# Optimization experiments

Hardware: AMD Instinct MI355X
Metric: run time of the kernel (lower is better)

The kernel has to match this reference:

```python
import jax, jax.numpy as jnp
import numpy as np


def setup_inputs() -> dict:
    key = jax.random.key(0)
    ks = jax.random.split(key, 7)
    B, C, H, W = 16, 256, 1, 4096
    x = jax.random.normal(ks[0], (B, C, H, W), dtype=jnp.float32)
    init = lambda k, s: jax.random.normal(k, s, dtype=jnp.float32) * 0.02
    return {
        "x": x,
        "Wq": init(ks[1], (C, C)), "bq": jnp.zeros((C,), jnp.float32),
        "Wk": init(ks[2], (C, C)), "bk": jnp.zeros((C,), jnp.float32),
        "Wv": init(ks[3], (C, C)), "bv": jnp.zeros((C,), jnp.float32),
    }


def reference(x, Wq, bq, Wk, bk, Wv, bv):
    B, C, H, W = x.shape
    xs = jnp.transpose(x[:, :, 0, :], (0, 2, 1))  # [B, W, C]
    Q = xs @ Wq.T + bq  # [B, W, C]
    K = xs @ Wk.T + bk
    V = xs @ Wv.T + bv
    scale = jnp.sqrt(jnp.asarray(C, dtype=Q.dtype))

    # radius-1 sliding window along width; pad so window gather is static
    Kp = jnp.pad(K, ((0, 0), (1, 1), (0, 0)))  # [B, W+2, C]
    Vp = jnp.pad(V, ((0, 0), (1, 1), (0, 0)))
    idx = jnp.arange(W)[:, None] + jnp.arange(3)[None, :]  # padded indices [W,3]
    pos = idx - 1  # original positions (may be -1 or W -> invalid at edges)
    valid = (pos >= 0) & (pos < W)  # [W, 3]

    Kw = Kp[:, idx]  # [B, W, 3, C]
    Vw = Vp[:, idx]  # [B, W, 3, C]

    scores = jnp.einsum('bwc,bwkc->bwk', Q, Kw) / scale  # [B, W, 3]
    scores = jnp.where(valid[None], scores, jnp.asarray(-1e9, scores.dtype))
    attn = jax.nn.softmax(scores, axis=-1)
    out = jnp.einsum('bwk,bwkc->bwc', attn, Vw)  # [B, W, C]
    # [B, W, C] -> [B, C, 1, W]
    return jnp.transpose(out, (0, 2, 1))[:, :, None, :]
```

## Files before the change

### kernel.cpp

```cpp
#include <hip/hip_runtime.h>
#include <hip/hip_bf16.h>

#define C_DIM 256
#define W_DIM 4096
#define LDS_BYTES 162528

typedef unsigned short u16;
typedef short s16x8 __attribute__((ext_vector_type(8)));
typedef unsigned short u16x8 __attribute__((ext_vector_type(8)));
typedef unsigned short u16x4 __attribute__((ext_vector_type(4)));
typedef float f32x16 __attribute__((ext_vector_type(16)));

__device__ __forceinline__ u16 f2b(float f) {
  return __builtin_bit_cast(u16, __float2bfloat16(f));
}
__device__ __forceinline__ float b2f(u16 u) {
  return __builtin_bit_cast(float, ((unsigned)u) << 16);
}

__global__ __launch_bounds__(256) void prep_kernel(
    const float* __restrict__ Wq, const float* __restrict__ bq,
    const float* __restrict__ Wk, const float* __restrict__ bk,
    const float* __restrict__ Wv, char* __restrict__ ws) {
  u16* Mb   = (u16*)ws;
  u16* Wvb  = (u16*)(ws + 131072);
  float* u0 = (float*)(ws + 262144);
  float* u1 = (float*)(ws + 263168);
  float* c0p = (float*)(ws + 264192);
  int bid = blockIdx.x, t = threadIdx.x;
  if (bid < 256) {
    __shared__ float Wqs[256*17];
    __shared__ float Wks[256*17];
    int i0 = (bid >> 4) << 4, j0 = (bid & 15) << 4;
    for (int it = 0; it < 16; ++it) {
      int e = t + 256*it; int a = e >> 4, ii = e & 15;
      Wqs[a*17+ii] = Wq[a*256 + i0 + ii];
      Wks[a*17+ii] = Wk[a*256 + j0 + ii];
    }
    __syncthreads();
    int ii = t >> 4, jj = t & 15;
    float acc = 0.f;
    #pragma unroll 8
    for (int a = 0; a < 256; ++a) acc += Wqs[a*17+ii] * Wks[a*17+jj];
    Mb[(i0+ii)*256 + j0 + jj] = f2b(acc);
  } else if (bid == 256) {
    int j = t;
    float a0 = 0.f, a1 = 0.f;
    #pragma unroll 4
    for (int a = 0; a < 256; ++a) {
      a0 += bq[a] * Wk[a*256 + j];
      a1 += bk[a] * Wq[a*256 + j];
    }
    u0[j] = a0; u1[j] = a1;
    __shared__ float red[256];
    red[t] = bq[t] * bk[t];
    __syncthreads();
    if (t == 0) { float s = 0.f; for (int a = 0; a < 256; ++a) s += red[a]; *c0p = s; }
  } else {
    int base = ((bid - 257)*256 + t) * 4;
    const float4 v = *reinterpret_cast<const float4*>(Wv + base);
    ushort4 pk = make_ushort4(f2b(v.x), f2b(v.y), f2b(v.z), f2b(v.w));
    *reinterpret_cast<ushort4*>(Wvb + base) = pk;
  }
}

__global__ __launch_bounds__(1024, 4) void main_kernel(
    const float* __restrict__ x, const char* __restrict__ ws,
    const float* __restrict__ bv, float* __restrict__ out) {
  const u16* Mb   = (const u16*)ws;
  const u16* Wvb  = (const u16*)(ws + 131072);
  const float* u0g = (const float*)(ws + 262144);
  const float* u1g = (const float*)(ws + 263168);
  const float c0  = *(const float*)(ws + 264192);

  extern __shared__ char lds[];
  u16*   Xt  = (u16*)lds;
  float* Ps  = (float*)(lds + 132608);
  float* ABs = (float*)(lds + 157376);
  float* fS  = (float*)(lds + 159440);
  float* U   = (float*)(lds + 159456);
  float* bvs = (float*)(lds + 161504);

  const int bid = blockIdx.x;
  const int t = threadIdx.x;
  const int wv = t >> 6, l = t & 63;
  const int col = l & 31, half = l >> 5;
  const int rg = wv & 7, nh = wv >> 3;
  const int nbase = 4*nh;
  const int kkA = 2*wv;

  const int b  = bid >> 4;
  const int cw = bid & 15;
  const int w0 = cw << 8;
  const float* xb = x + (size_t)b * (C_DIM*W_DIM);
  float* outb = out + (size_t)b * (C_DIM*W_DIM);

  for (int i = t; i < 6192; i += 1024) Ps[i] = 0.f;
  if (t < 4) fS[t] = 0.f;
  if (t < 256) { U[t] = u0g[t]; U[256+t] = u1g[t]; bvs[t] = bv[t]; }
  __syncthreads();

  {
    #pragma unroll
    for (int p = 0; p < 4; ++p) {
      int j = 64*p + l;
      int w = w0 - 1 + j;
      bool ok = (w >= 0);
      const float* xp = xb + w;
      float xr[16];
      #pragma unroll
      for (int g2 = 0; g2 < 2; ++g2)
        #pragma unroll
        for (int e = 0; e < 8; ++e)
          xr[g2*8+e] = ok ? xp[(size_t)((kkA+g2)*8 + e) * W_DIM] : 0.f;
      float pa = 0.f, pb_ = 0.f;
      #pragma unroll
      for (int g2 = 0; g2 < 2; ++g2) {
        int kk = kkA + g2;
        union { u16 u[8]; u16x8 v; } pk;
        #pragma unroll
        for (int e = 0; e < 8; ++e) {
          float v = xr[g2*8+e];
          pk.u[e] = f2b(v);
          int c = kk*8 + e;
          pa  += U[c] * v;
          pb_ += U[256 + c] * v;
        }
        *reinterpret_cast<u16x8*>(Xt + (kk*259 + j)*8) = pk.v;
      }
      atomicAdd(&Ps[rg*258 + j], pa);
      atomicAdd(&Ps[2064 + rg*258 + j], pb_);
    }
    if (l < 3) {
      int j = 256 + l;
      int w = w0 - 1 + j;
      bool real = (l < 2) && (w < W_DIM);
      const float* xpe = xb + w;
      float pa = 0.f, pb_ = 0.f;
      #pragma unroll
      for (int g2 = 0; g2 < 2; ++g2) {
        int kk = kkA + g2;
        union { u16 u[8]; u16x8 v; } pk;
        #pragma unroll
        for (int e = 0; e < 8; ++e) {
          float v = real ? xpe[(size_t)(kk*8+e) * W_DIM] : 0.f;
          pk.u[e] = f2b(v);
          int c = kk*8 + e;
          pa  += U[c] * v;
          pb_ += U[256 + c] * v;
        }
        *reinterpret_cast<u16x8*>(Xt + (kk*259 + j)*8) = pk.v;
      }
      if (l < 2) {
        atomicAdd(&Ps[rg*258 + j], pa);
        atomicAdd(&Ps[2064 + rg*258 + j], pb_);
      }
    }
  }
  __syncthreads();

  f32x16 acc[4];
  #pragma unroll
  for (int ni = 0; ni < 4; ++ni)
    #pragma unroll
    for (int r = 0; r < 16; ++r) acc[ni][r] = 0.f;
  {
    const u16* Arow = Mb + (32*rg + col)*256 + 8*half;
    #pragma unroll
    for (int kk = 0; kk < 16; ++kk) {
      s16x8 a = *reinterpret_cast<const s16x8*>(Arow + 16*kk);
      const u16* Bb = Xt + (2*kk + half)*259*8;
      #pragma unroll
      for (int ni = 0; ni < 4; ++ni) {
        s16x8 bfr = *reinterpret_cast<const s16x8*>(Bb + (32*(nbase+ni) + col)*8);
        acc[ni] = __builtin_amdgcn_mfma_f32_32x32x16_bf16(a, bfr, acc[ni], 0, 0, 0);
      }
    }
  }

  {
    int i = t >> 2, kq = t & 3;
    float xi255 = b2f(Xt[((i>>3)*259 + 255)*8 + (i&7)]);
    float xi256 = b2f(Xt[((i>>3)*259 + 256)*8 + (i&7)]);
    float a1 = 0.f, a2 = 0.f;
    const u16* Mrow = Mb + i*256 + 64*kq;
    #pragma unroll
    for (int kk8 = 0; kk8 < 8; ++kk8) {
      int sA = 8*kq + kk8;
      s16x8 m8 = *reinterpret_cast<const s16x8*>(Mrow + 8*kk8);
      u16x8 xk6 = *reinterpret_cast<const u16x8*>(Xt + (sA*259 + 256)*8);
      u16x8 xk7 = *reinterpret_cast<const u16x8*>(Xt + (sA*259 + 257)*8);
      #pragma unroll
      for (int e = 0; e < 8; ++e) {
        float m = b2f((u16)m8[e]);
        a1 += m * b2f(xk6[e]);
        a2 += m * b2f(xk7[e]);
      }
    }
    float p1 = xi256*a1, p2 = xi256*a2, p3 = xi255*a1;
    #pragma unroll
    for (int d = 1; d < 64; d <<= 1) {
      p1 += __shfl_xor(p1, d); p2 += __shfl_xor(p2, d); p3 += __shfl_xor(p3, d);
    }
    if (l == 0) { atomicAdd(&fS[0], p1); atomicAdd(&fS[1], p2); atomicAdd(&fS[2], p3); }
  }
  for (int i = t; i < 516; i += 1024) {
    int which = (i >= 258) ? 1 : 0;
    int jj = i - 258*which;
    float s = 0.f;
    #pragma unroll
    for (int g = 0; g < 8; ++g) s += Ps[which*2064 + g*258 + jj];
    ABs[which*258 + jj] = s;
  }
  __syncthreads();

  {
    #pragma unroll
    for (int ni = 0; ni < 4; ++ni) {
      int jt = 32*(nbase+ni) + col;
      int jm = (jt > 0) ? jt-1 : 0;
      int jp = jt + 1;
      float s0 = 0.f, s1 = 0.f, s2 = 0.f;
      #pragma unroll
      for (int q = 0; q < 4; ++q) {
        const u16* base = Xt + (4*rg + q)*259*8 + 4*half;
        u16x4 xm = *reinterpret_cast<const u16x4*>(base + jm*8);
        u16x4 xc = *reinterpret_cast<const u16x4*>(base + jt*8);
        u16x4 xp = *reinterpret_cast<const u16x4*>(base + jp*8);
        #pragma unroll
        for (int r4 = 0; r4 < 4; ++r4) {
          float g0 = acc[ni][4*q + r4];
          s2 += g0 * b2f(xm[r4]);
          s1 += g0 * b2f(xc[r4]);
          s0 += g0 * b2f(xp[r4]);
        }
      }
      s0 += __shfl_xor(s0, 32);
      s1 += __shfl_xor(s1, 32);
      s2 += __shfl_xor(s2, 32);
      if (half == 0) {
        Ps[0*2064 + rg*258 + jt+1] = s0;
        if (jt >= 1) Ps[1*2064 + rg*258 + jt]   = s1;
        if (jt >= 2) Ps[2*2064 + rg*258 + jt-1] = s2;
      }
    }
  }
  __syncthreads();

  {
    float aw0[4], aw1[4], aw2[4];
    #pragma unroll
    for (int p = 0; p < 4; ++p) {
      int oc = 64*p + l;
      int jp = oc + 1;
      float d0 = 0.f, d1 = 0.f, d2 = 0.f;
      #pragma unroll
      for (int g = 0; g < 8; ++g) {
        d0 += Ps[0*2064 + g*258 + jp];
        d1 += Ps[1*2064 + g*258 + jp];
        d2 += Ps[2*2064 + g*258 + jp];
      }
      if (oc == 255)      { d1 = fS[0]; d2 = fS[1]; }
      else if (oc == 254) { d2 = fS[2]; }
      float am = ABs[jp-1], ac_ = ABs[jp], ap_ = ABs[jp+1];
      float be = ABs[258 + jp];
      float sc0 = (d0 + am + be + c0) * 0.0625f;
      float sc1 = (d1 + ac_ + be + c0) * 0.0625f;
      float sc2 = (d2 + ap_ + be + c0) * 0.0625f;
      int w = w0 + oc;
      bool v0 = (w >= 1), v2 = (w + 1 < W_DIM);
      const float NEG = -1e30f;
      float m = fmaxf(v0 ? sc0 : NEG, fmaxf(sc1, v2 ? sc2 : NEG));
      float e0v = v0 ? __expf(sc0 - m) : 0.f;
      float e1v = __expf(sc1 - m);
      float e2v = v2 ? __expf(sc2 - m) : 0.f;
      float inv = 1.f / (e0v + e1v + e2v);
      aw0[p] = e0v*inv; aw1[p] = e1v*inv; aw2[p] = e2v*inv;
    }
    #pragma unroll
    for (int g2 = 0; g2 < 2; ++g2) {
      u16* base = Xt + (kkA + g2)*259*8;
      u16x8 xrd[12];
      #pragma unroll
      for (int p = 0; p < 4; ++p)
        #pragma unroll
        for (int i = 0; i < 3; ++i)
          xrd[p*3+i] = *reinterpret_cast<const u16x8*>(base + (64*p + l + i)*8);
      __builtin_amdgcn_sched_barrier(0);
      #pragma unroll
      for (int p = 0; p < 4; ++p) {
        union { u16 u[8]; u16x8 v; } pk;
        #pragma unroll
        for (int e = 0; e < 8; ++e)
          pk.u[e] = f2b(aw0[p]*b2f(xrd[p*3][e]) + aw1[p]*b2f(xrd[p*3+1][e])
                        + aw2[p]*b2f(xrd[p*3+2][e]));
        *reinterpret_cast<u16x8*>(base + (64*p + l + 1)*8) = pk.v;
      }
      __builtin_amdgcn_sched_barrier(0);
    }
  }
  __syncthreads();

  {
    #pragma unroll
    for (int ni = 0; ni < 4; ++ni)
      #pragma unroll
      for (int r = 0; r < 16; ++r) acc[ni][r] = 0.f;
    const u16* Arow2 = Wvb + (32*rg + col)*256 + 8*half;
    #pragma unroll
    for (int kk = 0; kk < 16; ++kk) {
      s16x8 a = *reinterpret_cast<const s16x8*>(Arow2 + 16*kk);
      const u16* Bb = Xt + (2*kk + half)*259*8;
      #pragma unroll
      for (int ni = 0; ni < 4; ++ni) {
        s16x8 bfr = *reinterpret_cast<const s16x8*>(Bb + (1 + 32*(nbase+ni) + col)*8);
        acc[ni] = __builtin_amdgcn_mfma_f32_32x32x16_bf16(a, bfr, acc[ni], 0, 0, 0);
      }
    }
    float bvr[16];
    #pragma unroll
    for (int q = 0; q < 4; ++q) {
      const float4 t4 = *reinterpret_cast<const float4*>(bvs + 32*rg + 8*q + 4*half);
      bvr[4*q+0] = t4.x; bvr[4*q+1] = t4.y; bvr[4*q+2] = t4.z; bvr[4*q+3] = t4.w;
    }
    #pragma unroll
    for (int ni = 0; ni < 4; ++ni)
      #pragma unroll
      for (int r = 0; r < 16; ++r) {
        int crow = 32*rg + (r&3) + 8*(r>>2) + 4*half;
        outb[(size_t)crow*W_DIM + w0 + 32*(nbase+ni) + col] = acc[ni][r] + bvr[r];
      }
  }
}

extern "C" void kernel_launch(void* const* d_in, const int* in_sizes, int n_in,
                              void* d_out, int out_size, void* d_ws, size_t ws_size,
                              hipStream_t stream) {
  (void)in_sizes; (void)n_in; (void)out_size; (void)ws_size;
  const float* x  = (const float*)d_in[0];
  const float* Wq = (const float*)d_in[1];
  const float* bq = (const float*)d_in[2];
  const float* Wk = (const float*)d_in[3];
  const float* bk = (const float*)d_in[4];
  const float* Wv = (const float*)d_in[5];
  const float* bv = (const float*)d_in[6];
  float* out = (float*)d_out;
  char* ws = (char*)d_ws;

  hipFuncSetAttribute((const void*)main_kernel,
                      hipFuncAttributeMaxDynamicSharedMemorySize, LDS_BYTES);
  prep_kernel<<<321, 256, 0, stream>>>(Wq, bq, Wk, bk, Wv, ws);
  main_kernel<<<256, 1024, LDS_BYTES, stream>>>(x, ws, bv, out);
}
```

Before: 87.93 us.

## Halve block size to 512 threads with 2x MFMA row tiles per wave

Main kernel now uses 8 waves instead of 16. Each wave computes two 32-row MFMA tiles that share one B fragment, and loads four channel groups of x instead of two. With 8 waves, each wave now writes its own partial-sum slot, so the LDS atomics and the Ps zeroing are removed. The change cuts LDS traffic for B fragments and the atomics, at the cost of fewer waves to hide latency, given that the LDS footprint already limits the kernel to one block per CU.

```diff
diff --git a/kernel.cpp b/kernel.cpp
--- a/kernel.cpp
+++ b/kernel.cpp
@@ -64,7 +64,7 @@
   }
 }
 
-__global__ __launch_bounds__(1024, 4) void main_kernel(
+__global__ __launch_bounds__(512, 2) void main_kernel(
     const float* __restrict__ x, const char* __restrict__ ws,
     const float* __restrict__ bv, float* __restrict__ out) {
   const u16* Mb   = (const u16*)ws;
@@ -85,9 +85,7 @@
   const int t = threadIdx.x;
   const int wv = t >> 6, l = t & 63;
   const int col = l & 31, half = l >> 5;
-  const int rg = wv & 7, nh = wv >> 3;
-  const int nbase = 4*nh;
-  const int kkA = 2*wv;
+  const int rs = wv & 3, cs = wv >> 2;
 
   const int b  = bid >> 4;
   const int cw = bid & 15;
@@ -95,7 +93,6 @@
   const float* xb = x + (size_t)b * (C_DIM*W_DIM);
   float* outb = out + (size_t)b * (C_DIM*W_DIM);
 
-  for (int i = t; i < 6192; i += 1024) Ps[i] = 0.f;
   if (t < 4) fS[t] = 0.f;
   if (t < 256) { U[t] = u0g[t]; U[256+t] = u1g[t]; bvs[t] = bv[t]; }
   __syncthreads();
@@ -107,29 +104,28 @@
       int w = w0 - 1 + j;
       bool ok = (w >= 0);
       const float* xp = xb + w;
-      float xr[16];
-      #pragma unroll
-      for (int g2 = 0; g2 < 2; ++g2)
+      float xr[32];
+      #pragma unroll
+      for (int g = 0; g < 4; ++g)
         #pragma unroll
         for (int e = 0; e < 8; ++e)
-          xr[g2*8+e] = ok ? xp[(size_t)((kkA+g2)*8 + e) * W_DIM] : 0.f;
+          xr[g*8+e] = ok ? xp[(size_t)((4*wv+g)*8 + e) * W_DIM] : 0.f;
       float pa = 0.f, pb_ = 0.f;
       #pragma unroll
-      for (int g2 = 0; g2 < 2; ++g2) {
-        int kk = kkA + g2;
+      for (int g = 0; g < 4; ++g) {
+        int kk = 4*wv + g;
         union { u16 u[8]; u16x8 v; } pk;
         #pragma unroll
         for (int e = 0; e < 8; ++e) {
-          float v = xr[g2*8+e];
+          float v = xr[g*8+e];
           pk.u[e] = f2b(v);
-          int c = kk*8 + e;
-          pa  += U[c] * v;
-          pb_ += U[256 + c] * v;
+          pa  += U[kk*8+e] * v;
+          pb_ += U[256 + kk*8+e] * v;
         }
         *reinterpret_cast<u16x8*>(Xt + (kk*259 + j)*8) = pk.v;
       }
-      atomicAdd(&Ps[rg*258 + j], pa);
-      atomicAdd(&Ps[2064 + rg*258 + j], pb_);
+      Ps[wv*258 + j] = pa;
+      Ps[2064 + wv*258 + j] = pb_;
     }
     if (l < 3) {
       int j = 256 + l;
@@ -138,55 +134,57 @@
       const float* xpe = xb + w;
       float pa = 0.f, pb_ = 0.f;
       #pragma unroll
-      for (int g2 = 0; g2 < 2; ++g2) {
-        int kk = kkA + g2;
+      for (int g = 0; g < 4; ++g) {
+        int kk = 4*wv + g;
         union { u16 u[8]; u16x8 v; } pk;
         #pragma unroll
         for (int e = 0; e < 8; ++e) {
           float v = real ? xpe[(size_t)(kk*8+e) * W_DIM] : 0.f;
           pk.u[e] = f2b(v);
-          int c = kk*8 + e;
-          pa  += U[c] * v;
-          pb_ += U[256 + c] * v;
+          pa  += U[kk*8+e] * v;
+          pb_ += U[256 + kk*8+e] * v;
         }
         *reinterpret_cast<u16x8*>(Xt + (kk*259 + j)*8) = pk.v;
       }
       if (l < 2) {
-        atomicAdd(&Ps[rg*258 + j], pa);
-        atomicAdd(&Ps[2064 + rg*258 + j], pb_);
-      }
-    }
-  }
-  __syncthreads();
-
-  f32x16 acc[4];
+        Ps[wv*258 + j] = pa;
+        Ps[2064 + wv*258 + j] = pb_;
+      }
+    }
+  }
+  __syncthreads();
+
+  f32x16 acc0[4], acc1[4];
   #pragma unroll
   for (int ni = 0; ni < 4; ++ni)
     #pragma unroll
-    for (int r = 0; r < 16; ++r) acc[ni][r] = 0.f;
-  {
-    const u16* Arow = Mb + (32*rg + col)*256 + 8*half;
+    for (int r = 0; r < 16; ++r) { acc0[ni][r] = 0.f; acc1[ni][r] = 0.f; }
+  {
+    const u16* Arow0 = Mb + (64*rs + col)*256 + 8*half;
+    const u16* Arow1 = Arow0 + 32*256;
     #pragma unroll
     for (int kk = 0; kk < 16; ++kk) {
-      s16x8 a = *reinterpret_cast<const s16x8*>(Arow + 16*kk);
+      s16x8 a0 = *reinterpret_cast<const s16x8*>(Arow0 + 16*kk);
+      s16x8 a1 = *reinterpret_cast<const s16x8*>(Arow1 + 16*kk);
       const u16* Bb = Xt + (2*kk + half)*259*8;
       #pragma unroll
       for (int ni = 0; ni < 4; ++ni) {
-        s16x8 bfr = *reinterpret_cast<const s16x8*>(Bb + (32*(nbase+ni) + col)*8);
-        acc[ni] = __builtin_amdgcn_mfma_f32_32x32x16_bf16(a, bfr, acc[ni], 0, 0, 0);
-      }
-    }
-  }
-
-  {
-    int i = t >> 2, kq = t & 3;
+        s16x8 bfr = *reinterpret_cast<const s16x8*>(Bb + (32*(4*cs+ni) + col)*8);
+        acc0[ni] = __builtin_amdgcn_mfma_f32_32x32x16_bf16(a0, bfr, acc0[ni], 0, 0, 0);
+        acc1[ni] = __builtin_amdgcn_mfma_f32_32x32x16_bf16(a1, bfr, acc1[ni], 0, 0, 0);
+      }
+    }
+  }
+
+  {
+    int i = t >> 1, kq = t & 1;
     float xi255 = b2f(Xt[((i>>3)*259 + 255)*8 + (i&7)]);
     float xi256 = b2f(Xt[((i>>3)*259 + 256)*8 + (i&7)]);
     float a1 = 0.f, a2 = 0.f;
-    const u16* Mrow = Mb + i*256 + 64*kq;
-    #pragma unroll
-    for (int kk8 = 0; kk8 < 8; ++kk8) {
-      int sA = 8*kq + kk8;
+    const u16* Mrow = Mb + i*256 + 128*kq;
+    #pragma unroll
+    for (int kk8 = 0; kk8 < 16; ++kk8) {
+      int sA = 16*kq + kk8;
       s16x8 m8 = *reinterpret_cast<const s16x8*>(Mrow + 8*kk8);
       u16x8 xk6 = *reinterpret_cast<const u16x8*>(Xt + (sA*259 + 256)*8);
       u16x8 xk7 = *reinterpret_cast<const u16x8*>(Xt + (sA*259 + 257)*8);
@@ -204,7 +202,7 @@
     }
     if (l == 0) { atomicAdd(&fS[0], p1); atomicAdd(&fS[1], p2); atomicAdd(&fS[2], p3); }
   }
-  for (int i = t; i < 516; i += 1024) {
+  for (int i = t; i < 516; i += 512) {
     int which = (i >= 258) ? 1 : 0;
     int jj = i - 258*which;
     float s = 0.f;
@@ -216,32 +214,37 @@
 
   {
     #pragma unroll
-    for (int ni = 0; ni < 4; ++ni) {
-      int jt = 32*(nbase+ni) + col;
-      int jm = (jt > 0) ? jt-1 : 0;
-      int jp = jt + 1;
-      float s0 = 0.f, s1 = 0.f, s2 = 0.f;
-      #pragma unroll
-      for (int q = 0; q < 4; ++q) {
-        const u16* base = Xt + (4*rg + q)*259*8 + 4*half;
-        u16x4 xm = *reinterpret_cast<const u16x4*>(base + jm*8);
-        u16x4 xc = *reinterpret_cast<const u16x4*>(base + jt*8);
-        u16x4 xp = *reinterpret_cast<const u16x4*>(base + jp*8);
-        #pragma unroll
-        for (int r4 = 0; r4 < 4; ++r4) {
-          float g0 = acc[ni][4*q + r4];
-          s2 += g0 * b2f(xm[r4]);
-          s1 += g0 * b2f(xc[r4]);
-          s0 += g0 * b2f(xp[r4]);
+    for (int rt = 0; rt < 2; ++rt) {
+      const int rg = 2*rs + rt;
+      #pragma unroll
+      for (int ni = 0; ni < 4; ++ni) {
+        int jt = 32*(4*cs+ni) + col;
+        int jm = (jt > 0) ? jt-1 : 0;
+        int jp = jt + 1;
+        float s0 = 0.f, s1 = 0.f, s2 = 0.f;
+        #pragma unroll
+        for (int q = 0; q < 4; ++q) {
+          const u16* base = Xt + (4*rg + q)*259*8 + 4*half;
+          u16x4 xm = *reinterpret_cast<const u16x4*>(base + jm*8);
+          u16x4 xc = *reinterpret_cast<const u16x4*>(base + jt*8);
+          u16x4 xp = *reinterpret_cast<const u16x4*>(base + jp*8);
+          const f32x16& A = rt ? acc1[ni] : acc0[ni];
+          #pragma unroll
+          for (int r4 = 0; r4 < 4; ++r4) {
+            float g0 = A[4*q + r4];
+            s2 += g0 * b2f(xm[r4]);
+            s1 += g0 * b2f(xc[r4]);
+            s0 += g0 * b2f(xp[r4]);
+          }
         }
-      }
-      s0 += __shfl_xor(s0, 32);
-      s1 += __shfl_xor(s1, 32);
-      s2 += __shfl_xor(s2, 32);
-      if (half == 0) {
-        Ps[0*2064 + rg*258 + jt+1] = s0;
-        if (jt >= 1) Ps[1*2064 + rg*258 + jt]   = s1;
-        if (jt >= 2) Ps[2*2064 + rg*258 + jt-1] = s2;
+        s0 += __shfl_xor(s0, 32);
+        s1 += __shfl_xor(s1, 32);
+        s2 += __shfl_xor(s2, 32);
+        if (half == 0) {
+          Ps[0*2064 + rg*258 + jt+1] = s0;
+          if (jt >= 1) Ps[1*2064 + rg*258 + jt]   = s1;
+          if (jt >= 2) Ps[2*2064 + rg*258 + jt-1] = s2;
+        }
       }
     }
   }
@@ -278,8 +281,8 @@
       aw0[p] = e0v*inv; aw1[p] = e1v*inv; aw2[p] = e2v*inv;
     }
     #pragma unroll
-    for (int g2 = 0; g2 < 2; ++g2) {
-      u16* base = Xt + (kkA + g2)*259*8;
+    for (int g = 0; g < 4; ++g) {
+      u16* base = Xt + (4*wv + g)*259*8;
       u16x8 xrd[12];
       #pragma unroll
       for (int p = 0; p < 4; ++p)
@@ -305,30 +308,31 @@
     #pragma unroll
     for (int ni = 0; ni < 4; ++ni)
       #pragma unroll
-      for (int r = 0; r < 16; ++r) acc[ni][r] = 0.f;
-    const u16* Arow2 = Wvb + (32*rg + col)*256 + 8*half;
+      for (int r = 0; r < 16; ++r) { acc0[ni][r] = 0.f; acc1[ni][r] = 0.f; }
+    const u16* Arow0 = Wvb + (64*rs + col)*256 + 8*half;
+    const u16* Arow1 = Arow0 + 32*256;
     #pragma unroll
     for (int kk = 0; kk < 16; ++kk) {
-      s16x8 a = *reinterpret_cast<const s16x8*>(Arow2 + 16*kk);
+      s16x8 a0 = *reinterpret_cast<const s16x8*>(Arow0 + 16*kk);
+      s16x8 a1 = *reinterpret_cast<const s16x8*>(Arow1 + 16*kk);
       const u16* Bb = Xt + (2*kk + half)*259*8;
       #pragma unroll
       for (int ni = 0; ni < 4; ++ni) {
-        s16x8 bfr = *reinterpret_cast<const s16x8*>(Bb + (1 + 32*(nbase+ni) + col)*8);
-        acc[ni] = __builtin_amdgcn_mfma_f32_32x32x16_bf16(a, bfr, acc[ni], 0, 0, 0);
-      }
-    }
-    float bvr[16];
-    #pragma unroll
-    for (int q = 0; q < 4; ++q) {
-      const float4 t4 = *reinterpret_cast<const float4*>(bvs + 32*rg + 8*q + 4*half);
-      bvr[4*q+0] = t4.x; bvr[4*q+1] = t4.y; bvr[4*q+2] = t4.z; bvr[4*q+3] = t4.w;
+        s16x8 bfr = *reinterpret_cast<const s16x8*>(Bb + (1 + 32*(4*cs+ni) + col)*8);
+        acc0[ni] = __builtin_amdgcn_mfma_f32_32x32x16_bf16(a0, bfr, acc0[ni], 0, 0, 0);
+        acc1[ni] = __builtin_amdgcn_mfma_f32_32x32x16_bf16(a1, bfr, acc1[ni], 0, 0, 0);
+      }
     }
     #pragma unroll
     for (int ni = 0; ni < 4; ++ni)
       #pragma unroll
       for (int r = 0; r < 16; ++r) {
-        int crow = 32*rg + (r&3) + 8*(r>>2) + 4*half;
-        outb[(size_t)crow*W_DIM + w0 + 32*(nbase+ni) + col] = acc[ni][r] + bvr[r];
+        int rloc = (r&3) + 8*(r>>2) + 4*half;
+        int crow0 = 64*rs + rloc;
+        int crow1 = crow0 + 32;
+        int oc = 32*(4*cs+ni) + col;
+        outb[(size_t)crow0*W_DIM + w0 + oc] = acc0[ni][r] + bvs[crow0];
+        outb[(size_t)crow1*W_DIM + w0 + oc] = acc1[ni][r] + bvs[crow1];
       }
   }
 }
@@ -350,5 +354,5 @@
   hipFuncSetAttribute((const void*)main_kernel,
                       hipFuncAttributeMaxDynamicSharedMemorySize, LDS_BYTES);
   prep_kernel<<<321, 256, 0, stream>>>(Wq, bq, Wk, bk, Wv, ws);
-  main_kernel<<<256, 1024, LDS_BYTES, stream>>>(x, ws, bv, out);
-}
+  main_kernel<<<256, 512, LDS_BYTES, stream>>>(x, ws, bv, out);
+}
```

New measurement: 84.43 us. -4.0%, faster.

## Halve width tile to 128 columns with 512-thread blocks and smaller LDS

Applied to the files above, without the earlier changes.

Each block now covers 128 width columns with 8 waves instead of 256 columns with 16 waves, so the grid doubles to 512 blocks and LDS use drops to about 77 KB. Each wave now owns a full 32-row channel slice across all four column tiles. Partial-sum buffers move from per-wave writes to atomic adds over 4 groups, with an extra zeroing pass and barrier. The aim is better occupancy (two blocks per CU fit in LDS) and more blocks to spread across CUs. The cost is twice as many halo columns and tail-correction computations, plus more LDS atomics.

```diff
diff --git a/kernel.cpp b/kernel.cpp
--- a/kernel.cpp
+++ b/kernel.cpp
@@ -3,7 +3,8 @@
 
 #define C_DIM 256
 #define W_DIM 4096
-#define LDS_BYTES 162528
+#define LDS_BYTES 76928
+#define XROW 1040
 
 typedef unsigned short u16;
 typedef short s16x8 __attribute__((ext_vector_type(8)));
@@ -64,7 +65,7 @@
   }
 }
 
-__global__ __launch_bounds__(1024, 4) void main_kernel(
+__global__ __launch_bounds__(512, 4) void main_kernel(
     const float* __restrict__ x, const char* __restrict__ ws,
     const float* __restrict__ bv, float* __restrict__ out) {
   const u16* Mb   = (const u16*)ws;
@@ -75,86 +76,84 @@
 
   extern __shared__ char lds[];
   u16*   Xt  = (u16*)lds;
-  float* Ps  = (float*)(lds + 132608);
-  float* ABs = (float*)(lds + 157376);
-  float* fS  = (float*)(lds + 159440);
-  float* U   = (float*)(lds + 159456);
-  float* bvs = (float*)(lds + 161504);
+  float* Ps  = (float*)(lds + 66560);
+  float* ABs = (float*)(lds + 72800);
+  float* fS  = (float*)(lds + 73840);
+  float* U   = (float*)(lds + 73856);
+  float* bvs = (float*)(lds + 75904);
 
   const int bid = blockIdx.x;
   const int t = threadIdx.x;
   const int wv = t >> 6, l = t & 63;
   const int col = l & 31, half = l >> 5;
-  const int rg = wv & 7, nh = wv >> 3;
-  const int nbase = 4*nh;
-  const int kkA = 2*wv;
-
-  const int b  = bid >> 4;
-  const int cw = bid & 15;
-  const int w0 = cw << 8;
+  const int g4 = wv & 3;
+  const int kkA = 4*wv;
+
+  const int b  = bid >> 5;
+  const int cw = bid & 31;
+  const int w0 = cw << 7;
   const float* xb = x + (size_t)b * (C_DIM*W_DIM);
   float* outb = out + (size_t)b * (C_DIM*W_DIM);
 
-  for (int i = t; i < 6192; i += 1024) Ps[i] = 0.f;
+  for (int i = t; i < 1560; i += 512) Ps[i] = 0.f;
   if (t < 4) fS[t] = 0.f;
   if (t < 256) { U[t] = u0g[t]; U[256+t] = u1g[t]; bvs[t] = bv[t]; }
   __syncthreads();
 
   {
     #pragma unroll
-    for (int p = 0; p < 4; ++p) {
+    for (int p = 0; p < 2; ++p) {
       int j = 64*p + l;
       int w = w0 - 1 + j;
       bool ok = (w >= 0);
       const float* xp = xb + w;
-      float xr[16];
-      #pragma unroll
-      for (int g2 = 0; g2 < 2; ++g2)
-        #pragma unroll
-        for (int e = 0; e < 8; ++e)
-          xr[g2*8+e] = ok ? xp[(size_t)((kkA+g2)*8 + e) * W_DIM] : 0.f;
       float pa = 0.f, pb_ = 0.f;
       #pragma unroll
-      for (int g2 = 0; g2 < 2; ++g2) {
-        int kk = kkA + g2;
-        union { u16 u[8]; u16x8 v; } pk;
-        #pragma unroll
-        for (int e = 0; e < 8; ++e) {
-          float v = xr[g2*8+e];
-          pk.u[e] = f2b(v);
-          int c = kk*8 + e;
-          pa  += U[c] * v;
-          pb_ += U[256 + c] * v;
+      for (int h = 0; h < 2; ++h) {
+        float xr[16];
+        #pragma unroll
+        for (int g2 = 0; g2 < 2; ++g2)
+          #pragma unroll
+          for (int e = 0; e < 8; ++e)
+            xr[g2*8+e] = ok ? xp[(size_t)((kkA+2*h+g2)*8 + e) * W_DIM] : 0.f;
+        #pragma unroll
+        for (int g2 = 0; g2 < 2; ++g2) {
+          int kk = kkA + 2*h + g2;
+          union { u16 u[8]; u16x8 v; } pk;
+          #pragma unroll
+          for (int e = 0; e < 8; ++e) {
+            float v = xr[g2*8+e];
+            pk.u[e] = f2b(v);
+            pa  += U[kk*8+e] * v;
+            pb_ += U[256 + kk*8+e] * v;
+          }
+          *reinterpret_cast<u16x8*>(Xt + kk*XROW + j*8) = pk.v;
         }
-        *reinterpret_cast<u16x8*>(Xt + (kk*259 + j)*8) = pk.v;
-      }
-      atomicAdd(&Ps[rg*258 + j], pa);
-      atomicAdd(&Ps[2064 + rg*258 + j], pb_);
-    }
-    if (l < 3) {
-      int j = 256 + l;
+      }
+      atomicAdd(&Ps[g4*130 + j], pa);
+      atomicAdd(&Ps[520 + g4*130 + j], pb_);
+    }
+    if (l < 2) {
+      int j = 128 + l;
       int w = w0 - 1 + j;
-      bool real = (l < 2) && (w < W_DIM);
+      bool real = (w < W_DIM);
       const float* xpe = xb + w;
       float pa = 0.f, pb_ = 0.f;
       #pragma unroll
-      for (int g2 = 0; g2 < 2; ++g2) {
-        int kk = kkA + g2;
+      for (int g = 0; g < 4; ++g) {
+        int kk = kkA + g;
         union { u16 u[8]; u16x8 v; } pk;
         #pragma unroll
         for (int e = 0; e < 8; ++e) {
           float v = real ? xpe[(size_t)(kk*8+e) * W_DIM] : 0.f;
           pk.u[e] = f2b(v);
-          int c = kk*8 + e;
-          pa  += U[c] * v;
-          pb_ += U[256 + c] * v;
+          pa  += U[kk*8+e] * v;
+          pb_ += U[256 + kk*8+e] * v;
         }
-        *reinterpret_cast<u16x8*>(Xt + (kk*259 + j)*8) = pk.v;
-      }
-      if (l < 2) {
-        atomicAdd(&Ps[rg*258 + j], pa);
-        atomicAdd(&Ps[2064 + rg*258 + j], pb_);
-      }
+        *reinterpret_cast<u16x8*>(Xt + kk*XROW + j*8) = pk.v;
+      }
+      atomicAdd(&Ps[g4*130 + j], pa);
+      atomicAdd(&Ps[520 + g4*130 + j], pb_);
     }
   }
   __syncthreads();
@@ -165,31 +164,31 @@
     #pragma unroll
     for (int r = 0; r < 16; ++r) acc[ni][r] = 0.f;
   {
-    const u16* Arow = Mb + (32*rg + col)*256 + 8*half;
+    const u16* Arow = Mb + (32*wv + col)*256 + 8*half;
     #pragma unroll
     for (int kk = 0; kk < 16; ++kk) {
       s16x8 a = *reinterpret_cast<const s16x8*>(Arow + 16*kk);
-      const u16* Bb = Xt + (2*kk + half)*259*8;
+      const u16* Bb = Xt + (2*kk + half)*XROW;
       #pragma unroll
       for (int ni = 0; ni < 4; ++ni) {
-        s16x8 bfr = *reinterpret_cast<const s16x8*>(Bb + (32*(nbase+ni) + col)*8);
+        s16x8 bfr = *reinterpret_cast<const s16x8*>(Bb + (32*ni + col)*8);
         acc[ni] = __builtin_amdgcn_mfma_f32_32x32x16_bf16(a, bfr, acc[ni], 0, 0, 0);
       }
     }
   }
 
   {
-    int i = t >> 2, kq = t & 3;
-    float xi255 = b2f(Xt[((i>>3)*259 + 255)*8 + (i&7)]);
-    float xi256 = b2f(Xt[((i>>3)*259 + 256)*8 + (i&7)]);
+    int i = t >> 1, kq = t & 1;
+    float xi127 = b2f(Xt[(i>>3)*XROW + 127*8 + (i&7)]);
+    float xi128 = b2f(Xt[(i>>3)*XROW + 128*8 + (i&7)]);
     float a1 = 0.f, a2 = 0.f;
-    const u16* Mrow = Mb + i*256 + 64*kq;
-    #pragma unroll
-    for (int kk8 = 0; kk8 < 8; ++kk8) {
-      int sA = 8*kq + kk8;
+    const u16* Mrow = Mb + i*256 + 128*kq;
+    #pragma unroll
+    for (int kk8 = 0; kk8 < 16; ++kk8) {
+      int sA = 16*kq + kk8;
       s16x8 m8 = *reinterpret_cast<const s16x8*>(Mrow + 8*kk8);
-      u16x8 xk6 = *reinterpret_cast<const u16x8*>(Xt + (sA*259 + 256)*8);
-      u16x8 xk7 = *reinterpret_cast<const u16x8*>(Xt + (sA*259 + 257)*8);
+      u16x8 xk6 = *reinterpret_cast<const u16x8*>(Xt + sA*XROW + 128*8);
+      u16x8 xk7 = *reinterpret_cast<const u16x8*>(Xt + sA*XROW + 129*8);
       #pragma unroll
       for (int e = 0; e < 8; ++e) {
         float m = b2f((u16)m8[e]);
@@ -197,33 +196,40 @@
         a2 += m * b2f(xk7[e]);
       }
     }
-    float p1 = xi256*a1, p2 = xi256*a2, p3 = xi255*a1;
+    float p1 = xi128*a1, p2 = xi128*a2, p3 = xi127*a1;
     #pragma unroll
     for (int d = 1; d < 64; d <<= 1) {
       p1 += __shfl_xor(p1, d); p2 += __shfl_xor(p2, d); p3 += __shfl_xor(p3, d);
     }
     if (l == 0) { atomicAdd(&fS[0], p1); atomicAdd(&fS[1], p2); atomicAdd(&fS[2], p3); }
   }
-  for (int i = t; i < 516; i += 1024) {
-    int which = (i >= 258) ? 1 : 0;
-    int jj = i - 258*which;
+  if (t < 260) {
+    int which = (t >= 130) ? 1 : 0;
+    int jj = t - 130*which;
     float s = 0.f;
     #pragma unroll
-    for (int g = 0; g < 8; ++g) s += Ps[which*2064 + g*258 + jj];
-    ABs[which*258 + jj] = s;
+    for (int g = 0; g < 4; ++g) s += Ps[which*520 + g*130 + jj];
+    ABs[which*130 + jj] = s;
+  }
+  __syncthreads();
+  if (t < 130) {
+    #pragma unroll
+    for (int pl = 0; pl < 3; ++pl)
+      #pragma unroll
+      for (int g = 0; g < 4; ++g) Ps[pl*520 + g*130 + t] = 0.f;
   }
   __syncthreads();
 
   {
     #pragma unroll
     for (int ni = 0; ni < 4; ++ni) {
-      int jt = 32*(nbase+ni) + col;
+      int jt = 32*ni + col;
       int jm = (jt > 0) ? jt-1 : 0;
       int jp = jt + 1;
       float s0 = 0.f, s1 = 0.f, s2 = 0.f;
       #pragma unroll
       for (int q = 0; q < 4; ++q) {
-        const u16* base = Xt + (4*rg + q)*259*8 + 4*half;
+        const u16* base = Xt + (kkA + q)*XROW + 4*half*1;
         u16x4 xm = *reinterpret_cast<const u16x4*>(base + jm*8);
         u16x4 xc = *reinterpret_cast<const u16x4*>(base + jt*8);
         u16x4 xp = *reinterpret_cast<const u16x4*>(base + jp*8);
@@ -239,31 +245,31 @@
       s1 += __shfl_xor(s1, 32);
       s2 += __shfl_xor(s2, 32);
       if (half == 0) {
-        Ps[0*2064 + rg*258 + jt+1] = s0;
-        if (jt >= 1) Ps[1*2064 + rg*258 + jt]   = s1;
-        if (jt >= 2) Ps[2*2064 + rg*258 + jt-1] = s2;
-      }
-    }
-  }
-  __syncthreads();
-
-  {
-    float aw0[4], aw1[4], aw2[4];
-    #pragma unroll
-    for (int p = 0; p < 4; ++p) {
+        atomicAdd(&Ps[0*520 + g4*130 + jt+1], s0);
+        if (jt >= 1) atomicAdd(&Ps[1*520 + g4*130 + jt], s1);
+        if (jt >= 2) atomicAdd(&Ps[2*520 + g4*130 + jt-1], s2);
+      }
+    }
+  }
+  __syncthreads();
+
+  {
+    float aw0[2], aw1[2], aw2[2];
+    #pragma unroll
+    for (int p = 0; p < 2; ++p) {
       int oc = 64*p + l;
       int jp = oc + 1;
       float d0 = 0.f, d1 = 0.f, d2 = 0.f;
       #pragma unroll
-      for (int g = 0; g < 8; ++g) {
-        d0 += Ps[0*2064 + g*258 + jp];
-        d1 += Ps[1*2064 + g*258 + jp];
-        d2 += Ps[2*2064 + g*258 + jp];
-      }
-      if (oc == 255)      { d1 = fS[0]; d2 = fS[1]; }
-      else if (oc == 254) { d2 = fS[2]; }
+      for (int g = 0; g < 4; ++g) {
+        d0 += Ps[0*520 + g*130 + jp];
+        d1 += Ps[1*520 + g*130 + jp];
+        d2 += Ps[2*520 + g*130 + jp];
+      }
+      if (oc == 127)      { d1 = fS[0]; d2 = fS[1]; }
+      else if (oc == 126) { d2 = fS[2]; }
       float am = ABs[jp-1], ac_ = ABs[jp], ap_ = ABs[jp+1];
-      float be = ABs[258 + jp];
+      float be = ABs[130 + jp];
       float sc0 = (d0 + am + be + c0) * 0.0625f;
       float sc1 = (d1 + ac_ + be + c0) * 0.0625f;
       float sc2 = (d2 + ap_ + be + c0) * 0.0625f;
@@ -278,17 +284,17 @@
       aw0[p] = e0v*inv; aw1[p] = e1v*inv; aw2[p] = e2v*inv;
     }
     #pragma unroll
-    for (int g2 = 0; g2 < 2; ++g2) {
-      u16* base = Xt + (kkA + g2)*259*8;
-      u16x8 xrd[12];
-      #pragma unroll
-      for (int p = 0; p < 4; ++p)
+    for (int g = 0; g < 4; ++g) {
+      u16* base = Xt + (kkA + g)*XROW;
+      u16x8 xrd[6];
+      #pragma unroll
+      for (int p = 0; p < 2; ++p)
         #pragma unroll
         for (int i = 0; i < 3; ++i)
           xrd[p*3+i] = *reinterpret_cast<const u16x8*>(base + (64*p + l + i)*8);
       __builtin_amdgcn_sched_barrier(0);
       #pragma unroll
-      for (int p = 0; p < 4; ++p) {
+      for (int p = 0; p < 2; ++p) {
         union { u16 u[8]; u16x8 v; } pk;
         #pragma unroll
         for (int e = 0; e < 8; ++e)
@@ -306,29 +312,23 @@
     for (int ni = 0; ni < 4; ++ni)
       #pragma unroll
       for (int r = 0; r < 16; ++r) acc[ni][r] = 0.f;
-    const u16* Arow2 = Wvb + (32*rg + col)*256 + 8*half;
+    const u16* Arow2 = Wvb + (32*wv + col)*256 + 8*half;
     #pragma unroll
     for (int kk = 0; kk < 16; ++kk) {
       s16x8 a = *reinterpret_cast<const s16x8*>(Arow2 + 16*kk);
-      const u16* Bb = Xt + (2*kk + half)*259*8;
+      const u16* Bb = Xt + (2*kk + half)*XROW;
       #pragma unroll
       for (int ni = 0; ni < 4; ++ni) {
-        s16x8 bfr = *reinterpret_cast<const s16x8*>(Bb + (1 + 32*(nbase+ni) + col)*8);
+        s16x8 bfr = *reinterpret_cast<const s16x8*>(Bb + (1 + 32*ni + col)*8);
         acc[ni] = __builtin_amdgcn_mfma_f32_32x32x16_bf16(a, bfr, acc[ni], 0, 0, 0);
       }
     }
-    float bvr[16];
-    #pragma unroll
-    for (int q = 0; q < 4; ++q) {
-      const float4 t4 = *reinterpret_cast<const float4*>(bvs + 32*rg + 8*q + 4*half);
-      bvr[4*q+0] = t4.x; bvr[4*q+1] = t4.y; bvr[4*q+2] = t4.z; bvr[4*q+3] = t4.w;
-    }
     #pragma unroll
     for (int ni = 0; ni < 4; ++ni)
       #pragma unroll
       for (int r = 0; r < 16; ++r) {
-        int crow = 32*rg + (r&3) + 8*(r>>2) + 4*half;
-        outb[(size_t)crow*W_DIM + w0 + 32*(nbase+ni) + col] = acc[ni][r] + bvr[r];
+        int crow = 32*wv + (r&3) + 8*(r>>2) + 4*half;
+        outb[(size_t)crow*W_DIM + w0 + 32*ni + col] = acc[ni][r] + bvs[crow];
       }
   }
 }
@@ -350,5 +350,5 @@
   hipFuncSetAttribute((const void*)main_kernel,
                       hipFuncAttributeMaxDynamicSharedMemorySize, LDS_BYTES);
   prep_kernel<<<321, 256, 0, stream>>>(Wq, bq, Wk, bk, Wv, ws);
-  main_kernel<<<256, 1024, LDS_BYTES, stream>>>(x, ws, bv, out);
-}
+  main_kernel<<<512, 512, LDS_BYTES, stream>>>(x, ws, bv, out);
+}
```

Result: slower. 93.54 us (+6.4%).
